# Kernel tuning notes

Hardware: AMD Instinct MI355X
Metric: run time of the kernel (lower is better)

Reference implementation:

```python
import jax, jax.numpy as jnp
import numpy as np

B, W, I, S, T, U, US = 4, 2000, 64, 64, 24, 32, 2
V, H, D, OUT = 32000, 4, 256, 512
PER = W + I + S + U + 1          # nodes per graph = 2161
N = B * PER                      # 8644 nodes
E_RAND = N * 16


def setup_inputs() -> dict:
    key = jax.random.key(0)
    ks = jax.random.split(key, 24)
    s = 0.02
    inp = {}
    inp["all_words"] = jax.random.randint(ks[0], (B * W,), 0, V)
    inp["image_feats"] = jax.random.normal(ks[1], (B * I, 2048), jnp.float32)
    inp["sentences"] = jax.random.randint(ks[2], (B, S, T), 0, V)
    inp["sentence_mask"] = jnp.ones((B, S, T), jnp.float32)
    inp["utterances"] = jax.random.randint(ks[3], (B, U, US), 0, S)
    inp["utterance_mask"] = jnp.ones((B, U, US), jnp.float32)
    inp["session_ids"] = (jnp.arange(B) + 1) * PER - 1   # last node of each graph
    src = jax.random.randint(ks[4], (E_RAND,), 0, N)
    dst = jax.random.randint(ks[5], (E_RAND,), 0, N)
    loop = jnp.arange(N)
    inp["edge_src"] = jnp.concatenate([src, loop])
    inp["edge_dst"] = jnp.concatenate([dst, loop])
    # learned parameters
    inp["word_embed"] = jax.random.normal(ks[6], (V, 300), jnp.float32) * s
    inp["text_fc_w"] = jax.random.normal(ks[7], (300, 1024), jnp.float32) * s
    inp["text_fc_b"] = jnp.zeros((1024,), jnp.float32)
    inp["image_fc_w"] = jax.random.normal(ks[8], (2048, 1024), jnp.float32) * s
    inp["image_fc_b"] = jnp.zeros((1024,), jnp.float32)
    inp["gat0_fc"] = jax.random.normal(ks[9], (1024, H * D), jnp.float32) * s
    inp["gat0_al"] = jax.random.normal(ks[10], (H, D), jnp.float32) * s
    inp["gat0_ar"] = jax.random.normal(ks[11], (H, D), jnp.float32) * s
    inp["gat0_b"] = jnp.zeros((H * D,), jnp.float32)
    inp["gat1_fc"] = jax.random.normal(ks[12], (H * D, H * D), jnp.float32) * s
    inp["gat1_al"] = jax.random.normal(ks[13], (H, D), jnp.float32) * s
    inp["gat1_ar"] = jax.random.normal(ks[14], (H, D), jnp.float32) * s
    inp["gat1_b"] = jnp.zeros((H * D,), jnp.float32)
    inp["gat2_fc"] = jax.random.normal(ks[15], (H * D, OUT), jnp.float32) * s
    inp["gat2_al"] = jax.random.normal(ks[16], (1, OUT), jnp.float32) * s
    inp["gat2_ar"] = jax.random.normal(ks[17], (1, OUT), jnp.float32) * s
    inp["gat2_b"] = jnp.zeros((OUT,), jnp.float32)
    return inp


def _gat_layer(h, src, dst, fc_w, al, ar, b, act):
    # DGL GATConv: fc -> per-head attention logits -> edge softmax over dst -> aggregate
    n = h.shape[0]
    nh, dd = al.shape
    f = (h @ fc_w).reshape(n, nh, dd)                    # [N,H,D]
    el = (f * al).sum(-1)                                # [N,H]
    er = (f * ar).sum(-1)
    e = jax.nn.leaky_relu(el[src] + er[dst], 0.2)        # [E,H]
    m = jax.ops.segment_max(e, dst, num_segments=n)      # stable softmax per dst node
    a = jnp.exp(e - m[dst])
    z = jax.ops.segment_sum(a, dst, num_segments=n)
    alpha = a / z[dst]                                   # [E,H]
    out = jax.ops.segment_sum(alpha[:, :, None] * f[src], dst, num_segments=n)
    out = out + b.reshape(nh, dd)
    if act:
        out = jax.nn.elu(out)
    return out.reshape(n, nh * dd)


def _masked_mean(x, mask):
    # x: [..., K, F], mask: [..., K]
    s = (x * mask[..., None]).sum(-2)
    cnt = mask.sum(-1, keepdims=True)
    cnt = jnp.where(cnt == 0, 1.0, cnt)
    return s / cnt


def reference(all_words, image_feats, sentences, sentence_mask, utterances,
              utterance_mask, session_ids, edge_src, edge_dst,
              word_embed, text_fc_w, text_fc_b, image_fc_w, image_fc_b,
              gat0_fc, gat0_al, gat0_ar, gat0_b,
              gat1_fc, gat1_al, gat1_ar, gat1_b,
              gat2_fc, gat2_al, gat2_ar, gat2_b):
    b, s_num, t_num = sentences.shape
    u_num, us_num = utterances.shape[1], utterances.shape[2]
    w_per = all_words.shape[0] // b
    i_per = image_feats.shape[0] // b

    # word nodes
    we = word_embed[all_words].reshape(b, w_per, 300)
    # sentence nodes: masked mean over words
    sw = word_embed[sentences]                           # [B,S,T,300]
    sent = _masked_mean(sw, sentence_mask)               # [B,S,300]
    # utterance nodes: gather sentence embeds, masked mean over sentences
    uidx = utterances.reshape(b, u_num * us_num)
    ue = jnp.take_along_axis(sent, uidx[:, :, None], axis=1).reshape(b, u_num, us_num, -1)
    utt = _masked_mean(ue, utterance_mask)               # [B,U,300]
    # session node
    sess = utt.mean(axis=1, keepdims=True)               # [B,1,300]

    txt = lambda x: x @ text_fc_w + text_fc_b
    wf, sf, uf, ssf = txt(we), txt(sent), txt(utt), txt(sess)
    imf = (image_feats @ image_fc_w + image_fc_b).reshape(b, i_per, -1)

    # node layout per graph: [words, images, sentences, utterances, session]
    h = jnp.concatenate([wf, imf, sf, uf, ssf], axis=1).reshape(-1, 1024)

    h = _gat_layer(h, edge_src, edge_dst, gat0_fc, gat0_al, gat0_ar, gat0_b, act=True)
    h = _gat_layer(h, edge_src, edge_dst, gat1_fc, gat1_al, gat1_ar, gat1_b, act=True)
    h = _gat_layer(h, edge_src, edge_dst, gat2_fc, gat2_al, gat2_ar, gat2_b, act=False)

    return h[session_ids]                                # [B, 512]
```

## Files before the change

kernel.cpp:

```cpp
#include <hip/hip_runtime.h>
#include <math.h>

constexpr int kB = 4, kW = 2000, kI = 64, kS = 64, kT = 24, kU = 32, kUS = 2;
constexpr int kPER = kW + kI + kS + kU + 1;
constexpr int kN   = kB * kPER;
constexpr int kTxtPer  = kW + kS + kU + 1;
constexpr int kTxtRows = kB * kTxtPer;
constexpr int kEmb = 300;
constexpr int kEmbPad = 320;
constexpr int kHid = 1024;
constexpr int kOut = 512;
constexpr int kCap = 256;
constexpr int kMaxDeg = 256;

typedef __attribute__((ext_vector_type(8))) short bf16x8;
typedef __attribute__((ext_vector_type(4))) float f32x4;

__device__ __forceinline__ unsigned short f2bf(float f) {
  union { float f; unsigned int u; } x; x.f = f;
  unsigned int r = x.u + 0x7FFF + ((x.u >> 16) & 1);
  return (unsigned short)(r >> 16);
}
__device__ __forceinline__ float bf2f(unsigned short u) {
  union { unsigned int u; float f; } x; x.u = ((unsigned int)u) << 16;
  return x.f;
}


__global__ void k_sent(const int* __restrict__ sents, const float* __restrict__ smask,
                       const float* __restrict__ wemb, float* __restrict__ sent) {
  int bs = blockIdx.x;
  __shared__ int idx[kT];
  __shared__ float mk[kT];
  __shared__ float s_cnt;
  int t = threadIdx.x;
  if (t < kT) { idx[t] = sents[bs * kT + t]; mk[t] = smask[bs * kT + t]; }
  __syncthreads();
  if (t == 0) {
    float c = 0.f;
    for (int i = 0; i < kT; ++i) c += mk[i];
    s_cnt = (c == 0.f) ? 1.f : c;
  }
  __syncthreads();
  for (int d = t; d < kEmb; d += blockDim.x) {
    float acc = 0.f;
    for (int i = 0; i < kT; ++i) acc += wemb[idx[i] * kEmb + d] * mk[i];
    sent[bs * kEmb + d] = acc / s_cnt;
  }
}

__global__ void k_utt(const int* __restrict__ utts, const float* __restrict__ umask,
                      const float* __restrict__ sent, float* __restrict__ utt) {
  int bu = blockIdx.x;
  int b = bu / kU;
  __shared__ int idx[kUS];
  __shared__ float mk[kUS];
  __shared__ float s_cnt;
  int t = threadIdx.x;
  if (t < kUS) { idx[t] = utts[bu * kUS + t]; mk[t] = umask[bu * kUS + t]; }
  __syncthreads();
  if (t == 0) {
    float c = 0.f;
    for (int i = 0; i < kUS; ++i) c += mk[i];
    s_cnt = (c == 0.f) ? 1.f : c;
  }
  __syncthreads();
  for (int d = t; d < kEmb; d += blockDim.x) {
    float acc = 0.f;
    for (int i = 0; i < kUS; ++i) acc += sent[(b * kS + idx[i]) * kEmb + d] * mk[i];
    utt[bu * kEmb + d] = acc / s_cnt;
  }
}

__global__ void k_sess(const float* __restrict__ utt, float* __restrict__ sess) {
  int b = blockIdx.x;
  for (int d = threadIdx.x; d < kEmb; d += blockDim.x) {
    float acc = 0.f;
    for (int u = 0; u < kU; ++u) acc += utt[(b * kU + u) * kEmb + d];
    sess[b * kEmb + d] = acc * (1.f / kU);
  }
}

__global__ void k_txtgather(const int* __restrict__ aw, const float* __restrict__ wemb,
                            const float* __restrict__ sent, const float* __restrict__ utt,
                            const float* __restrict__ sess, unsigned short* __restrict__ txt) {
  int r = blockIdx.x;
  int g = r / kTxtPer, j = r - g * kTxtPer;
  const float* src;
  if (j < kW)                 src = wemb + (size_t)aw[g * kW + j] * kEmb;
  else if (j < kW + kS)       src = sent + (size_t)(g * kS + (j - kW)) * kEmb;
  else if (j < kW + kS + kU)  src = utt  + (size_t)(g * kU + (j - kW - kS)) * kEmb;
  else                        src = sess + (size_t)g * kEmb;
  for (int d = threadIdx.x; d < kEmbPad; d += blockDim.x)
    txt[(size_t)r * kEmbPad + d] = (d < kEmb) ? f2bf(src[d]) : (unsigned short)0;
}

__global__ void k_rowmap(int* __restrict__ rt, int* __restrict__ ri) {
  int i = blockIdx.x * blockDim.x + threadIdx.x;
  if (i < kTxtRows) {
    int g = i / kTxtPer, j = i - g * kTxtPer;
    int base = g * kPER;
    int node;
    if (j < kW)                 node = base + j;
    else if (j < kW + kS)       node = base + kW + kI + (j - kW);
    else if (j < kW + kS + kU)  node = base + kW + kI + kS + (j - kW - kS);
    else                        node = base + kW + kI + kS + kU;
    rt[i] = node;
  }
  if (i < kB * kI) {
    int g = i >> 6;
    ri[i] = g * kPER + kW + (i & 63);
  }
}

__global__ void k_prep(const float* __restrict__ tx_w, unsigned short* __restrict__ o_tx,
                       const float* __restrict__ im_w, unsigned short* __restrict__ o_im,
                       const float* __restrict__ g0_w, unsigned short* __restrict__ o_g0,
                       const float* __restrict__ g1_w, unsigned short* __restrict__ o_g1,
                       const float* __restrict__ g2_w, unsigned short* __restrict__ o_g2,
                       const float* __restrict__ img, unsigned short* __restrict__ o_img) {
  int b = blockIdx.x;
  int tx = threadIdx.x, ty = threadIdx.y;
  const float* in; unsigned short* out; int K, N, Kpad, nbx;
  if (b < 320)               { in = tx_w; out = o_tx; K = kEmb; N = kHid; Kpad = kEmbPad; nbx = 32; }
  else if ((b -= 320) < 2048){ in = im_w; out = o_im; K = 2048; N = kHid; Kpad = 2048; nbx = 32; }
  else if ((b -= 2048) < 1024){ in = g0_w; out = o_g0; K = kHid; N = kHid; Kpad = kHid; nbx = 32; }
  else if ((b -= 1024) < 1024){ in = g1_w; out = o_g1; K = kHid; N = kHid; Kpad = kHid; nbx = 32; }
  else if ((b -= 1024) < 512) { in = g2_w; out = o_g2; K = kHid; N = kOut; Kpad = kHid; nbx = 16; }
  else {
    int i = (b - 512) * 1024 + (ty * 32 + tx) * 4;
    float4 v = *(const float4*)(img + i);
    ushort4 o; o.x = f2bf(v.x); o.y = f2bf(v.y); o.z = f2bf(v.z); o.w = f2bf(v.w);
    *(ushort4*)(o_img + i) = o;
    return;
  }
  int bx = b % nbx, by = b / nbx;
  __shared__ float t[32][33];
  int n = bx * 32 + tx;
#pragma unroll
  for (int j = 0; j < 4; ++j) {
    int k = by * 32 + ty + j * 8;
    t[ty + j * 8][tx] = (k < K) ? in[(size_t)k * N + n] : 0.f;
  }
  __syncthreads();
#pragma unroll
  for (int j = 0; j < 4; ++j) {
    int nn = bx * 32 + ty + j * 8;
    int kk = by * 32 + tx;
    out[(size_t)nn * Kpad + kk] = f2bf(t[tx][ty + j * 8]);
  }
}

template <bool OBF>
__global__ __launch_bounds__(256) void k_mm2(const unsigned short* __restrict__ A,
                                             const unsigned short* __restrict__ Bt,
                                             const float* __restrict__ bias,
                                             const int* __restrict__ rmap,
                                             void* __restrict__ Cout,
                                             int M, int K, int Nc) {
  __shared__ __align__(16) unsigned short As[128 * 64];
  __shared__ __align__(16) unsigned short Bs[128 * 64];
  int nCol = Nc >> 7;
  int bi = blockIdx.x;
  int xcd = bi & 7, bj = bi >> 3;
  int colTile = bj % nCol;
  int rowTile = ((bj / nCol) << 3) + xcd;
  int row0 = rowTile << 7;
  if (row0 >= M) return;
  int col0 = colTile << 7;

  int tid = threadIdx.x;
  int wid = tid >> 6, lane = tid & 63, quad = lane >> 4, l16 = lane & 15;
  int wm = wid >> 1, wn = wid & 1;

  f32x4 acc[4][4];
  f32x4 zero4 = {0.f, 0.f, 0.f, 0.f};
#pragma unroll
  for (int i = 0; i < 4; ++i)
#pragma unroll
    for (int j = 0; j < 4; ++j) acc[i][j] = zero4;

  int ar_ = tid >> 3;
  int ac = tid & 7;

  for (int k0 = 0; k0 < K; k0 += 64) {
    __syncthreads();
#pragma unroll
    for (int i = 0; i < 4; ++i) {
      int r = ar_ + i * 32;
      int sw = ((ac ^ (r & 7)) << 3);
      int grow = row0 + r;
      uint4 va = make_uint4(0u, 0u, 0u, 0u);
      if (grow < M) va = *(const uint4*)(A + (size_t)grow * K + k0 + ac * 8);
      *(uint4*)&As[r * 64 + sw] = va;
      int nrow = col0 + r;
      uint4 vb = *(const uint4*)(Bt + (size_t)nrow * K + k0 + ac * 8);
      *(uint4*)&Bs[r * 64 + sw] = vb;
    }
    __syncthreads();
#pragma unroll
    for (int s = 0; s < 2; ++s) {
      int cc = s * 4 + quad;
      bf16x8 aF[4], bF[4];
#pragma unroll
      for (int mi = 0; mi < 4; ++mi) {
        int r = wm * 64 + mi * 16 + l16;
        aF[mi] = *(const bf16x8*)&As[r * 64 + ((cc ^ (r & 7)) << 3)];
      }
#pragma unroll
      for (int ni = 0; ni < 4; ++ni) {
        int r = wn * 64 + ni * 16 + l16;
        bF[ni] = *(const bf16x8*)&Bs[r * 64 + ((cc ^ (r & 7)) << 3)];
      }
#pragma unroll
      for (int mi = 0; mi < 4; ++mi)
#pragma unroll
        for (int ni = 0; ni < 4; ++ni)
          acc[mi][ni] = __builtin_amdgcn_mfma_f32_16x16x32_bf16(aF[mi], bF[ni], acc[mi][ni], 0, 0, 0);
    }
  }

#pragma unroll
  for (int mi = 0; mi < 4; ++mi) {
#pragma unroll
    for (int ni = 0; ni < 4; ++ni) {
      int gm0 = row0 + wm * 64 + mi * 16 + quad * 4;
      int gn  = col0 + wn * 64 + ni * 16 + l16;
      float bv = bias ? bias[gn] : 0.f;
#pragma unroll
      for (int i = 0; i < 4; ++i) {
        int r = gm0 + i;
        if (r >= M) continue;
        float v = acc[mi][ni][i] + bv;
        if (OBF) {
          int orow = rmap ? rmap[r] : r;
          ((unsigned short*)Cout)[(size_t)orow * Nc + gn] = f2bf(v);
        } else {
          ((float*)Cout)[(size_t)r * Nc + gn] = v;
        }
      }
    }
  }
}

__global__ void k_elr4(const unsigned short* __restrict__ f, const float* __restrict__ al,
                       const float* __restrict__ ar, float* __restrict__ el,
                       float* __restrict__ er) {
  int v = blockIdx.x;
  int h = threadIdx.x >> 6, lane = threadIdx.x & 63;
  int d = lane * 4;
  ushort4 fv = *(const ushort4*)(f + (size_t)v * 1024 + h * 256 + d);
  float4 av = *(const float4*)(al + h * 256 + d);
  float4 rv = *(const float4*)(ar + h * 256 + d);
  float x0 = bf2f(fv.x), x1 = bf2f(fv.y), x2 = bf2f(fv.z), x3 = bf2f(fv.w);
  float a = x0 * av.x + x1 * av.y + x2 * av.z + x3 * av.w;
  float b = x0 * rv.x + x1 * rv.y + x2 * rv.z + x3 * rv.w;
#pragma unroll
  for (int off = 32; off; off >>= 1) {
    a += __shfl_down(a, off);
    b += __shfl_down(b, off);
  }
  if (lane == 0) { el[v * 4 + h] = a; er[v * 4 + h] = b; }
}

__global__ __launch_bounds__(256) void k_mm_sk(const unsigned short* __restrict__ A,
                                               const unsigned short* __restrict__ Bt,
                                               const int* __restrict__ rowlist,
                                               float* __restrict__ C,
                                               int M, int K, int Nc, int Kc) {
  __shared__ __align__(16) unsigned short As[64 * 64];
  __shared__ __align__(16) unsigned short Bs[64 * 64];
  int tid = threadIdx.x;
  int wid = tid >> 6, lane = tid & 63, quad = lane >> 4, l16 = lane & 15;
  int row0 = blockIdx.y * 64, col0 = blockIdx.x * 64;
  int k0 = blockIdx.z * Kc;
  int k1 = k0 + Kc; if (k1 > K) k1 = K;

  f32x4 acc[4];
  f32x4 zero4 = {0.f, 0.f, 0.f, 0.f};
#pragma unroll
  for (int i = 0; i < 4; ++i) acc[i] = zero4;

  int ar_ = tid >> 3;
  int ac = tid & 7;

  for (int kk = k0; kk < k1; kk += 64) {
    __syncthreads();
#pragma unroll
    for (int i = 0; i < 2; ++i) {
      int r = ar_ + i * 32;
      int sw = ((ac ^ (r & 7)) << 3);
      int grow = row0 + r;
      uint4 va = make_uint4(0u, 0u, 0u, 0u);
      if (grow < M) {
        int arow = rowlist ? rowlist[grow] : grow;
        va = *(const uint4*)(A + (size_t)arow * K + kk + ac * 8);
      }
      *(uint4*)&As[r * 64 + sw] = va;
      int nrow = col0 + r;
      uint4 vb = *(const uint4*)(Bt + (size_t)nrow * K + kk + ac * 8);
      *(uint4*)&Bs[r * 64 + sw] = vb;
    }
    __syncthreads();
#pragma unroll
    for (int s = 0; s < 2; ++s) {
      int cc = s * 4 + quad;
      bf16x8 bF;
      {
        int r = wid * 16 + l16;
        bF = *(const bf16x8*)&Bs[r * 64 + ((cc ^ (r & 7)) << 3)];
      }
#pragma unroll
      for (int mi = 0; mi < 4; ++mi) {
        int r = mi * 16 + l16;
        bf16x8 aF = *(const bf16x8*)&As[r * 64 + ((cc ^ (r & 7)) << 3)];
        acc[mi] = __builtin_amdgcn_mfma_f32_16x16x32_bf16(aF, bF, acc[mi], 0, 0, 0);
      }
    }
  }
#pragma unroll
  for (int mi = 0; mi < 4; ++mi) {
#pragma unroll
    for (int i = 0; i < 4; ++i) {
      int r = row0 + mi * 16 + quad * 4 + i;
      int c = col0 + wid * 16 + l16;
      if (r < M) atomicAdd(&C[(size_t)r * Nc + c], acc[mi][i]);
    }
  }
}

__global__ void k_sk_epi(const float* __restrict__ Cw, const float* __restrict__ bias,
                         const int* __restrict__ rmap, unsigned short* __restrict__ out,
                         int M, int Nc) {
  int i = blockIdx.x * blockDim.x + threadIdx.x;
  if (i >= M * Nc) return;
  int r = i / Nc, c = i - r * Nc;
  out[(size_t)rmap[r] * Nc + c] = f2bf(Cw[i] + bias[c]);
}

__global__ void k_count(const int* __restrict__ dst, int* __restrict__ cnt, int E) {
  int e = blockIdx.x * blockDim.x + threadIdx.x;
  if (e < E) atomicAdd(&cnt[dst[e]], 1);
}

__global__ void k_scan(const int* __restrict__ deg, int* __restrict__ offs, int n) {
  __shared__ int part[1024];
  int tid = threadIdx.x;
  int per = (n + 1023) >> 10;
  int start = tid * per;
  int local = 0;
  for (int i = 0; i < per; ++i) { int idx = start + i; if (idx < n) local += deg[idx]; }
  part[tid] = local;
  __syncthreads();
  for (int off = 1; off < 1024; off <<= 1) {
    int add = (tid >= off) ? part[tid - off] : 0;
    __syncthreads();
    part[tid] += add;
    __syncthreads();
  }
  int run = (tid == 0) ? 0 : part[tid - 1];
  for (int i = 0; i < per; ++i) {
    int idx = start + i;
    if (idx < n) { offs[idx] = run; run += deg[idx]; }
  }
  if (tid == 1023) offs[n] = part[1023];
}

__global__ void k_fill(const int* __restrict__ src, const int* __restrict__ dst,
                       const int* __restrict__ offs, int* __restrict__ cur,
                       int* __restrict__ csr, int E) {
  int e = blockIdx.x * blockDim.x + threadIdx.x;
  if (e < E) {
    int d = dst[e];
    int slot = offs[d] + atomicAdd(&cur[d], 1);
    csr[slot] = src[e];
  }
}

__global__ __launch_bounds__(256) void k_agg3(const unsigned short* __restrict__ f,
                                              const float* __restrict__ el,
                                              const float* __restrict__ er,
                                              const int* __restrict__ offs,
                                              const int* __restrict__ csr,
                                              const float* __restrict__ bias,
                                              unsigned short* __restrict__ out) {
  __shared__ float xs[4][kMaxDeg];
  int v = blockIdx.x;
  int tid = threadIdx.x;
  int h = tid >> 6, lane = tid & 63;
  int e0 = offs[v];
  int deg = offs[v + 1] - e0;
  if (deg > kMaxDeg) deg = kMaxDeg;

  float erv = er[v * 4 + h];
  float m = -1e30f;
  for (int base = 0; base < deg; base += 64) {
    int idx = base + lane;
    float x = -1e30f;
    if (idx < deg) {
      int s = csr[e0 + idx];
      x = el[s * 4 + h] + erv;
      x = x > 0.f ? x : 0.2f * x;
      xs[h][idx] = x;
    }
    float mm = x;
#pragma unroll
    for (int o = 32; o; o >>= 1) mm = fmaxf(mm, __shfl_xor(mm, o));
    m = fmaxf(m, mm);
  }
  float zs = 0.f;
  for (int base = 0; base < deg; base += 64) {
    int idx = base + lane;
    if (idx < deg) {
      float w = expf(xs[h][idx] - m);
      xs[h][idx] = w;
      zs += w;
    }
  }
#pragma unroll
  for (int o = 32; o; o >>= 1) zs += __shfl_xor(zs, o);
  float rz = 1.f / zs;
  for (int base = 0; base < deg; base += 64) {
    int idx = base + lane;
    if (idx < deg) xs[h][idx] *= rz;
  }
  __syncthreads();

  int d0 = tid * 4;
  float a0 = 0.f, a1 = 0.f, a2 = 0.f, a3 = 0.f;
  for (int e = 0; e < deg; ++e) {
    int s = csr[e0 + e];
    float w = xs[h][e];
    ushort4 fv = *(const ushort4*)(f + (size_t)s * 1024 + d0);
    a0 += w * bf2f(fv.x);
    a1 += w * bf2f(fv.y);
    a2 += w * bf2f(fv.z);
    a3 += w * bf2f(fv.w);
  }
  float4 bv = *(const float4*)(bias + d0);
  float o0 = a0 + bv.x, o1 = a1 + bv.y, o2 = a2 + bv.z, o3 = a3 + bv.w;
  o0 = o0 > 0.f ? o0 : expm1f(o0);
  o1 = o1 > 0.f ? o1 : expm1f(o1);
  o2 = o2 > 0.f ? o2 : expm1f(o2);
  o3 = o3 > 0.f ? o3 : expm1f(o3);
  ushort4 ov;
  ov.x = f2bf(o0); ov.y = f2bf(o1); ov.z = f2bf(o2); ov.w = f2bf(o3);
  *(ushort4*)(out + (size_t)v * 1024 + d0) = ov;
}

__global__ void k_rows2(const int* __restrict__ sid, const int* __restrict__ offs,
                        const int* __restrict__ csr, int* __restrict__ rowlist,
                        int* __restrict__ info) {
  __shared__ int degs[kB], starts[kB], total;
  int tid = threadIdx.x;
  int bv = tid >> 6, lane = tid & 63;
  if (tid < kB) {
    int v = sid[tid];
    degs[tid] = offs[v + 1] - offs[v];
  }
  __syncthreads();
  if (tid == 0) {
    int p = 0;
    for (int b = 0; b < kB; ++b) {
      starts[b] = p;
      int d = degs[b];
      if (p + d > kCap) d = kCap - p;
      degs[b] = d;
      p += d;
    }
    total = p;
  }
  __syncthreads();
  int v = sid[bv];
  int e0 = offs[v];
  int deg = degs[bv];
  int start = starts[bv];
  if (lane == 0) {
    info[bv] = start;
    info[4 + bv] = deg;
    info[8 + bv] = start;
  }
  __syncthreads();
  for (int idx = lane; idx < deg; idx += 64) {
    int s = csr[e0 + idx];
    rowlist[start + idx] = s;
    if (s == v) info[8 + bv] = start + idx;
  }
  for (int i = total + tid; i < kCap; i += 256) rowlist[i] = 0;
}

__global__ void k_elr_c(const float* __restrict__ fc, const float* __restrict__ al,
                        const float* __restrict__ ar, float* __restrict__ el,
                        float* __restrict__ er) {
  int r = blockIdx.x;
  int lane = threadIdx.x;
  float a = 0.f, b = 0.f;
  for (int d = lane * 4; d < 512; d += 256) {
    float4 x = *(const float4*)(fc + (size_t)r * 512 + d);
    float4 av = *(const float4*)(al + d);
    float4 rv = *(const float4*)(ar + d);
    a += x.x * av.x + x.y * av.y + x.z * av.z + x.w * av.w;
    b += x.x * rv.x + x.y * rv.y + x.z * rv.z + x.w * rv.w;
  }
#pragma unroll
  for (int off = 32; off; off >>= 1) {
    a += __shfl_down(a, off);
    b += __shfl_down(b, off);
  }
  if (lane == 0) { el[r] = a; er[r] = b; }
}

__global__ __launch_bounds__(256) void k_agg_fin2(const float* __restrict__ fc,
                                                  const float* __restrict__ el,
                                                  const float* __restrict__ er,
                                                  const int* __restrict__ info,
                                                  const float* __restrict__ bias,
                                                  float* __restrict__ out) {
  int bv = blockIdx.x;
  int tid = threadIdx.x;
  int start = info[bv], cnt = info[4 + bv];
  float erv = er[info[8 + bv]];
  float m = -1e30f;
  for (int i = 0; i < cnt; ++i) {
    float x = el[start + i] + erv;
    x = x > 0.f ? x : 0.2f * x;
    m = fmaxf(m, x);
  }
  float z = 0.f, a0 = 0.f, a1 = 0.f;
  for (int i = 0; i < cnt; ++i) {
    int r = start + i;
    float x = el[r] + erv;
    x = x > 0.f ? x : 0.2f * x;
    float w = expf(x - m);
    z += w;
    a0 += w * fc[(size_t)r * 512 + tid];
    a1 += w * fc[(size_t)r * 512 + 256 + tid];
  }
  out[bv * 512 + tid] = a0 / z + bias[tid];
  out[bv * 512 + 256 + tid] = a1 / z + bias[256 + tid];
}

extern "C" void kernel_launch(void* const* d_in, const int* in_sizes, int n_in,
                              void* d_out, int out_size, void* d_ws, size_t ws_size,
                              hipStream_t stream) {
  const int*   all_words   = (const int*)d_in[0];
  const float* image_feats = (const float*)d_in[1];
  const int*   sentences   = (const int*)d_in[2];
  const float* sent_mask   = (const float*)d_in[3];
  const int*   utterances  = (const int*)d_in[4];
  const float* utt_mask    = (const float*)d_in[5];
  const int*   session_ids = (const int*)d_in[6];
  const int*   edge_src    = (const int*)d_in[7];
  const int*   edge_dst    = (const int*)d_in[8];
  const float* word_embed  = (const float*)d_in[9];
  const float* text_fc_w   = (const float*)d_in[10];
  const float* text_fc_b   = (const float*)d_in[11];
  const float* image_fc_w  = (const float*)d_in[12];
  const float* image_fc_b  = (const float*)d_in[13];
  const float* gat0_fc     = (const float*)d_in[14];
  const float* gat0_al     = (const float*)d_in[15];
  const float* gat0_ar     = (const float*)d_in[16];
  const float* gat0_b      = (const float*)d_in[17];
  const float* gat1_fc     = (const float*)d_in[18];
  const float* gat1_al     = (const float*)d_in[19];
  const float* gat1_ar     = (const float*)d_in[20];
  const float* gat1_b      = (const float*)d_in[21];
  const float* gat2_fc     = (const float*)d_in[22];
  const float* gat2_al     = (const float*)d_in[23];
  const float* gat2_ar     = (const float*)d_in[24];
  const float* gat2_b      = (const float*)d_in[25];

  const int E = in_sizes[7];

  char* base = (char*)d_ws;
  size_t off = 0;
  auto alloc = [&](size_t elems, size_t esz) -> void* {
    void* p = base + off;
    off += ((elems * esz + 255) / 256) * 256;
    return p;
  };
  unsigned short* Abf   = (unsigned short*)alloc((size_t)kN * kHid, 2);
  unsigned short* fbf   = (unsigned short*)alloc((size_t)kN * kHid, 2);
  unsigned short* txtbf = (unsigned short*)alloc((size_t)kTxtRows * kEmbPad, 2);
  unsigned short* imgbf = (unsigned short*)alloc((size_t)kB * kI * 2048, 2);
  unsigned short* wtTx  = (unsigned short*)alloc((size_t)kHid * kEmbPad, 2);
  unsigned short* wtIm  = (unsigned short*)alloc((size_t)kHid * 2048, 2);
  unsigned short* wtG0  = (unsigned short*)alloc((size_t)kHid * kHid, 2);
  unsigned short* wtG1  = (unsigned short*)alloc((size_t)kHid * kHid, 2);
  unsigned short* wtG2  = (unsigned short*)alloc((size_t)kOut * kHid, 2);
  float* Cimg   = (float*)alloc((size_t)kB * kI * kHid, 4);
  float* Cg2    = (float*)alloc((size_t)kCap * kOut, 4);
  float* sentb  = (float*)alloc((size_t)kB * kS * kEmb, 4);
  float* uttb   = (float*)alloc((size_t)kB * kU * kEmb, 4);
  float* sessb  = (float*)alloc((size_t)kB * kEmb, 4);
  float* el     = (float*)alloc((size_t)kN * 4, 4);
  float* er     = (float*)alloc((size_t)kN * 4, 4);
  int*   offs   = (int*)alloc(kN + 1, 4);
  int*   cnt    = (int*)alloc(kN, 4);
  int*   csr    = (int*)alloc(E, 4);
  int*   rmt    = (int*)alloc(kTxtRows, 4);
  int*   rmi    = (int*)alloc(kB * kI, 4);
  int*   rowl   = (int*)alloc(kCap, 4);
  int*   info   = (int*)alloc(16, 4);
  (void)ws_size; (void)n_in; (void)out_size;

  k_sent<<<kB * kS, 128, 0, stream>>>(sentences, sent_mask, word_embed, sentb);
  k_utt<<<kB * kU, 128, 0, stream>>>(utterances, utt_mask, sentb, uttb);
  k_sess<<<kB, 128, 0, stream>>>(uttb, sessb);
  k_txtgather<<<kTxtRows, 128, 0, stream>>>(all_words, word_embed, sentb, uttb, sessb, txtbf);
  k_rowmap<<<(kTxtRows + 255) / 256, 256, 0, stream>>>(rmt, rmi);
  k_prep<<<5440, dim3(32, 8), 0, stream>>>(text_fc_w, wtTx, image_fc_w, wtIm,
                                           gat0_fc, wtG0, gat1_fc, wtG1, gat2_fc, wtG2,
                                           image_feats, imgbf);

  hipMemsetAsync(cnt, 0, kN * sizeof(int), stream);
  k_count<<<(E + 255) / 256, 256, 0, stream>>>(edge_dst, cnt, E);
  k_scan<<<1, 1024, 0, stream>>>(cnt, offs, kN);
  hipMemsetAsync(cnt, 0, kN * sizeof(int), stream);
  k_fill<<<(E + 255) / 256, 256, 0, stream>>>(edge_src, edge_dst, offs, cnt, csr, E);

  auto mmGrid = [](int M, int Nc) {
    int nrt = (M + 127) / 128;
    return 8 * (Nc / 128) * ((nrt + 7) / 8);
  };

  k_mm2<true><<<mmGrid(kTxtRows, kHid), 256, 0, stream>>>(
      txtbf, wtTx, text_fc_b, rmt, Abf, kTxtRows, kEmbPad, kHid);

  hipMemsetAsync(Cimg, 0, (size_t)kB * kI * kHid * sizeof(float), stream);
  k_mm_sk<<<dim3(kHid / 64, kB * kI / 64, 4), 256, 0, stream>>>(
      imgbf, wtIm, nullptr, Cimg, kB * kI, 2048, kHid, 512);
  k_sk_epi<<<(kB * kI * kHid + 255) / 256, 256, 0, stream>>>(
      Cimg, image_fc_b, rmi, Abf, kB * kI, kHid);

  k_mm2<true><<<mmGrid(kN, kHid), 256, 0, stream>>>(
      Abf, wtG0, nullptr, nullptr, fbf, kN, kHid, kHid);
  k_elr4<<<kN, 256, 0, stream>>>(fbf, gat0_al, gat0_ar, el, er);
  k_agg3<<<kN, 256, 0, stream>>>(fbf, el, er, offs, csr, gat0_b, Abf);

  k_mm2<true><<<mmGrid(kN, kHid), 256, 0, stream>>>(
      Abf, wtG1, nullptr, nullptr, fbf, kN, kHid, kHid);
  k_elr4<<<kN, 256, 0, stream>>>(fbf, gat1_al, gat1_ar, el, er);
  k_agg3<<<kN, 256, 0, stream>>>(fbf, el, er, offs, csr, gat1_b, Abf);

  k_rows2<<<1, 256, 0, stream>>>(session_ids, offs, csr, rowl, info);
  hipMemsetAsync(Cg2, 0, (size_t)kCap * kOut * sizeof(float), stream);
  k_mm_sk<<<dim3(kOut / 64, kCap / 64, 4), 256, 0, stream>>>(
      Abf, wtG2, rowl, Cg2, kCap, kHid, kOut, 256);
  k_elr_c<<<kCap, 64, 0, stream>>>(Cg2, gat2_al, gat2_ar, el, er);
  k_agg_fin2<<<kB, 256, 0, stream>>>(Cg2, el, er, info, gat2_b, (float*)d_out);
}
```

Measured before the change: 444.0 us.

## Fold attention projections into GEMM columns and merge small setup kernels

Precomputes W·a_l and W·a_r as eight extra weight columns so the GAT layer-0/1 GEMMs emit el/er directly, removing the separate k_elr4 passes over the features. Merges the sentence, rowmap, memset and weight-prep work into one large prep kernel, fuses utterance/session and text-gather/edge-count kernels, and moves the count reset into the scan. This cuts launch count and one read of the feature matrix per layer. In exchange the GEMMs gain a ninth column tile that is mostly padding, and el/er are computed from bf16 weights instead of bf16 features, which changes rounding.

```diff
diff --git a/kernel.cpp b/kernel.cpp
--- a/kernel.cpp
+++ b/kernel.cpp
@@ -12,6 +12,7 @@
 constexpr int kOut = 512;
 constexpr int kCap = 256;
 constexpr int kMaxDeg = 256;
+constexpr int kNcB = 1152;
 
 typedef __attribute__((ext_vector_type(8))) short bf16x8;
 typedef __attribute__((ext_vector_type(4))) float f32x4;
@@ -26,114 +27,105 @@
   return x.f;
 }
 
-
-__global__ void k_sent(const int* __restrict__ sents, const float* __restrict__ smask,
-                       const float* __restrict__ wemb, float* __restrict__ sent) {
-  int bs = blockIdx.x;
-  __shared__ int idx[kT];
-  __shared__ float mk[kT];
-  __shared__ float s_cnt;
-  int t = threadIdx.x;
-  if (t < kT) { idx[t] = sents[bs * kT + t]; mk[t] = smask[bs * kT + t]; }
-  __syncthreads();
-  if (t == 0) {
-    float c = 0.f;
-    for (int i = 0; i < kT; ++i) c += mk[i];
-    s_cnt = (c == 0.f) ? 1.f : c;
-  }
-  __syncthreads();
-  for (int d = t; d < kEmb; d += blockDim.x) {
-    float acc = 0.f;
-    for (int i = 0; i < kT; ++i) acc += wemb[idx[i] * kEmb + d] * mk[i];
-    sent[bs * kEmb + d] = acc / s_cnt;
-  }
-}
-
-__global__ void k_utt(const int* __restrict__ utts, const float* __restrict__ umask,
-                      const float* __restrict__ sent, float* __restrict__ utt) {
-  int bu = blockIdx.x;
-  int b = bu / kU;
-  __shared__ int idx[kUS];
-  __shared__ float mk[kUS];
-  __shared__ float s_cnt;
-  int t = threadIdx.x;
-  if (t < kUS) { idx[t] = utts[bu * kUS + t]; mk[t] = umask[bu * kUS + t]; }
-  __syncthreads();
-  if (t == 0) {
-    float c = 0.f;
-    for (int i = 0; i < kUS; ++i) c += mk[i];
-    s_cnt = (c == 0.f) ? 1.f : c;
-  }
-  __syncthreads();
-  for (int d = t; d < kEmb; d += blockDim.x) {
-    float acc = 0.f;
-    for (int i = 0; i < kUS; ++i) acc += sent[(b * kS + idx[i]) * kEmb + d] * mk[i];
-    utt[bu * kEmb + d] = acc / s_cnt;
-  }
-}
-
-__global__ void k_sess(const float* __restrict__ utt, float* __restrict__ sess) {
+__global__ __launch_bounds__(256) void k_prep0(
+    const float* __restrict__ tx_w, unsigned short* __restrict__ o_tx,
+    const float* __restrict__ im_w, unsigned short* __restrict__ o_im,
+    const float* __restrict__ g0_w, unsigned short* __restrict__ o_g0,
+    const float* __restrict__ g1_w, unsigned short* __restrict__ o_g1,
+    const float* __restrict__ g2_w, unsigned short* __restrict__ o_g2,
+    const float* __restrict__ img, unsigned short* __restrict__ o_img,
+    const int* __restrict__ sents, const float* __restrict__ smask,
+    const float* __restrict__ wemb, float* __restrict__ sent,
+    int* __restrict__ rmt, int* __restrict__ rmi,
+    int* __restrict__ cnt, float* __restrict__ Cimg, float* __restrict__ Cg2,
+    const float* __restrict__ g0_al, const float* __restrict__ g0_ar,
+    const float* __restrict__ g1_al, const float* __restrict__ g1_ar) {
   int b = blockIdx.x;
-  for (int d = threadIdx.x; d < kEmb; d += blockDim.x) {
-    float acc = 0.f;
-    for (int u = 0; u < kU; ++u) acc += utt[(b * kU + u) * kEmb + d];
-    sess[b * kEmb + d] = acc * (1.f / kU);
-  }
-}
-
-__global__ void k_txtgather(const int* __restrict__ aw, const float* __restrict__ wemb,
-                            const float* __restrict__ sent, const float* __restrict__ utt,
-                            const float* __restrict__ sess, unsigned short* __restrict__ txt) {
-  int r = blockIdx.x;
-  int g = r / kTxtPer, j = r - g * kTxtPer;
-  const float* src;
-  if (j < kW)                 src = wemb + (size_t)aw[g * kW + j] * kEmb;
-  else if (j < kW + kS)       src = sent + (size_t)(g * kS + (j - kW)) * kEmb;
-  else if (j < kW + kS + kU)  src = utt  + (size_t)(g * kU + (j - kW - kS)) * kEmb;
-  else                        src = sess + (size_t)g * kEmb;
-  for (int d = threadIdx.x; d < kEmbPad; d += blockDim.x)
-    txt[(size_t)r * kEmbPad + d] = (d < kEmb) ? f2bf(src[d]) : (unsigned short)0;
-}
-
-__global__ void k_rowmap(int* __restrict__ rt, int* __restrict__ ri) {
-  int i = blockIdx.x * blockDim.x + threadIdx.x;
-  if (i < kTxtRows) {
-    int g = i / kTxtPer, j = i - g * kTxtPer;
-    int base = g * kPER;
-    int node;
-    if (j < kW)                 node = base + j;
-    else if (j < kW + kS)       node = base + kW + kI + (j - kW);
-    else if (j < kW + kS + kU)  node = base + kW + kI + kS + (j - kW - kS);
-    else                        node = base + kW + kI + kS + kU;
-    rt[i] = node;
-  }
-  if (i < kB * kI) {
-    int g = i >> 6;
-    ri[i] = g * kPER + kW + (i & 63);
-  }
-}
-
-__global__ void k_prep(const float* __restrict__ tx_w, unsigned short* __restrict__ o_tx,
-                       const float* __restrict__ im_w, unsigned short* __restrict__ o_im,
-                       const float* __restrict__ g0_w, unsigned short* __restrict__ o_g0,
-                       const float* __restrict__ g1_w, unsigned short* __restrict__ o_g1,
-                       const float* __restrict__ g2_w, unsigned short* __restrict__ o_g2,
-                       const float* __restrict__ img, unsigned short* __restrict__ o_img) {
-  int b = blockIdx.x;
-  int tx = threadIdx.x, ty = threadIdx.y;
-  const float* in; unsigned short* out; int K, N, Kpad, nbx;
-  if (b < 320)               { in = tx_w; out = o_tx; K = kEmb; N = kHid; Kpad = kEmbPad; nbx = 32; }
-  else if ((b -= 320) < 2048){ in = im_w; out = o_im; K = 2048; N = kHid; Kpad = 2048; nbx = 32; }
+  int tid = threadIdx.x;
+  int tx = tid & 31, ty = tid >> 5;
+
+  const float* in = nullptr; unsigned short* out = nullptr; int K = 0, N = 0, Kpad = 0, nbx = 0;
+  if (b < 320)                { in = tx_w; out = o_tx; K = kEmb; N = kHid; Kpad = kEmbPad; nbx = 32; }
+  else if ((b -= 320) < 2048) { in = im_w; out = o_im; K = 2048; N = kHid; Kpad = 2048; nbx = 32; }
   else if ((b -= 2048) < 1024){ in = g0_w; out = o_g0; K = kHid; N = kHid; Kpad = kHid; nbx = 32; }
   else if ((b -= 1024) < 1024){ in = g1_w; out = o_g1; K = kHid; N = kHid; Kpad = kHid; nbx = 32; }
   else if ((b -= 1024) < 512) { in = g2_w; out = o_g2; K = kHid; N = kOut; Kpad = kHid; nbx = 16; }
-  else {
-    int i = (b - 512) * 1024 + (ty * 32 + tx) * 4;
+  else if ((b -= 512) < 512) {
+    int i = b * 1024 + tid * 4;
     float4 v = *(const float4*)(img + i);
     ushort4 o; o.x = f2bf(v.x); o.y = f2bf(v.y); o.z = f2bf(v.z); o.w = f2bf(v.w);
     *(ushort4*)(o_img + i) = o;
     return;
-  }
+  } else if ((b -= 512) < 256) {
+    __shared__ int idx[kT];
+    __shared__ float mk[kT];
+    __shared__ float s_cnt;
+    if (tid < kT) { idx[tid] = sents[b * kT + tid]; mk[tid] = smask[b * kT + tid]; }
+    __syncthreads();
+    if (tid == 0) {
+      float c = 0.f;
+      for (int i = 0; i < kT; ++i) c += mk[i];
+      s_cnt = (c == 0.f) ? 1.f : c;
+    }
+    __syncthreads();
+    for (int d = tid; d < kEmb; d += 256) {
+      float acc = 0.f;
+      for (int i = 0; i < kT; ++i) acc += wemb[idx[i] * kEmb + d] * mk[i];
+      sent[b * kEmb + d] = acc / s_cnt;
+    }
+    return;
+  } else if ((b -= 256) < 34) {
+    int i = b * 256 + tid;
+    if (i < kTxtRows) {
+      int g = i / kTxtPer, j = i - g * kTxtPer;
+      int base = g * kPER;
+      int node;
+      if (j < kW)                 node = base + j;
+      else if (j < kW + kS)       node = base + kW + kI + (j - kW);
+      else if (j < kW + kS + kU)  node = base + kW + kI + kS + (j - kW - kS);
+      else                        node = base + kW + kI + kS + kU;
+      rmt[i] = node;
+    }
+    if (i < kB * kI) {
+      int g = i >> 6;
+      rmi[i] = g * kPER + kW + (i & 63);
+    }
+    return;
+  } else if ((b -= 34) < 34) {
+    int i = b * 256 + tid;
+    if (i < kN) cnt[i] = 0;
+    return;
+  } else if ((b -= 34) < 256) {
+    uint4 z = make_uint4(0u, 0u, 0u, 0u);
+    ((uint4*)Cimg)[b * 256 + tid] = z;
+    return;
+  } else if ((b -= 256) < 128) {
+    uint4 z = make_uint4(0u, 0u, 0u, 0u);
+    ((uint4*)Cg2)[b * 256 + tid] = z;
+    return;
+  } else if ((b -= 128) < 8) {
+    int layer = b >> 2, which = (b >> 1) & 1, kslab = b & 1;
+    const float* fc = layer ? g1_w : g0_w;
+    const float* a  = layer ? (which ? g1_ar : g1_al) : (which ? g0_ar : g0_al);
+    unsigned short* wt = layer ? o_g1 : o_g0;
+    for (int k = kslab * 512 + tid; k < kslab * 512 + 512; k += 256) {
+#pragma unroll
+      for (int h = 0; h < 4; ++h) {
+        float s = 0.f;
+        for (int d = 0; d < 256; ++d) s += fc[(size_t)k * kHid + h * 256 + d] * a[h * 256 + d];
+        wt[(size_t)(1024 + which * 4 + h) * kHid + k] = f2bf(s);
+      }
+    }
+    return;
+  } else {
+    b -= 8;
+    int i = b * 256 + tid;
+    uint4 z = make_uint4(0u, 0u, 0u, 0u);
+    ((uint4*)(o_g0 + (size_t)1032 * kHid))[i] = z;
+    ((uint4*)(o_g1 + (size_t)1032 * kHid))[i] = z;
+    return;
+  }
+
   int bx = b % nbx, by = b / nbx;
   __shared__ float t[32][33];
   int n = bx * 32 + tx;
@@ -151,16 +143,90 @@
   }
 }
 
-template <bool OBF>
+__global__ __launch_bounds__(256) void k_utt_sess(const int* __restrict__ utts,
+                                                  const float* __restrict__ umask,
+                                                  const float* __restrict__ sent,
+                                                  float* __restrict__ utt,
+                                                  float* __restrict__ sess) {
+  int blk = blockIdx.x;
+  int tid = threadIdx.x;
+  if (blk < kB * kU) {
+    int bu = blk, b = bu / kU;
+    __shared__ int idx[kUS];
+    __shared__ float mk[kUS];
+    __shared__ float s_cnt;
+    if (tid < kUS) { idx[tid] = utts[bu * kUS + tid]; mk[tid] = umask[bu * kUS + tid]; }
+    __syncthreads();
+    if (tid == 0) {
+      float c = 0.f;
+      for (int i = 0; i < kUS; ++i) c += mk[i];
+      s_cnt = (c == 0.f) ? 1.f : c;
+    }
+    __syncthreads();
+    for (int d = tid; d < kEmb; d += 256) {
+      float acc = 0.f;
+      for (int i = 0; i < kUS; ++i) acc += sent[(b * kS + idx[i]) * kEmb + d] * mk[i];
+      utt[bu * kEmb + d] = acc / s_cnt;
+    }
+  } else {
+    int b = blk - kB * kU;
+    for (int d = tid; d < kEmb; d += 256) {
+      float acc = 0.f;
+      for (int u = 0; u < kU; ++u) {
+        float ua = 0.f, c = 0.f;
+        for (int us = 0; us < kUS; ++us) {
+          int i = (b * kU + u) * kUS + us;
+          int sidx = utts[i];
+          float m = umask[i];
+          ua += sent[(b * kS + sidx) * kEmb + d] * m;
+          c += m;
+        }
+        if (c == 0.f) c = 1.f;
+        acc += ua / c;
+      }
+      sess[b * kEmb + d] = acc * (1.f / kU);
+    }
+  }
+}
+
+__global__ __launch_bounds__(256) void k_txtcount(const int* __restrict__ aw,
+                                                  const float* __restrict__ wemb,
+                                                  const float* __restrict__ sent,
+                                                  const float* __restrict__ utt,
+                                                  const float* __restrict__ sess,
+                                                  unsigned short* __restrict__ txt,
+                                                  const int* __restrict__ dst,
+                                                  int* __restrict__ cnt, int E) {
+  int blk = blockIdx.x;
+  int tid = threadIdx.x;
+  if (blk < kTxtRows) {
+    int r = blk;
+    int g = r / kTxtPer, j = r - g * kTxtPer;
+    const float* src;
+    if (j < kW)                 src = wemb + (size_t)aw[g * kW + j] * kEmb;
+    else if (j < kW + kS)       src = sent + (size_t)(g * kS + (j - kW)) * kEmb;
+    else if (j < kW + kS + kU)  src = utt  + (size_t)(g * kU + (j - kW - kS)) * kEmb;
+    else                        src = sess + (size_t)g * kEmb;
+    for (int d = tid; d < kEmbPad; d += 256)
+      txt[(size_t)r * kEmbPad + d] = (d < kEmb) ? f2bf(src[d]) : (unsigned short)0;
+  } else {
+    int e = (blk - kTxtRows) * 256 + tid;
+    if (e < E) atomicAdd(&cnt[dst[e]], 1);
+  }
+}
+
+template <bool OBF, bool ELR>
 __global__ __launch_bounds__(256) void k_mm2(const unsigned short* __restrict__ A,
                                              const unsigned short* __restrict__ Bt,
                                              const float* __restrict__ bias,
                                              const int* __restrict__ rmap,
                                              void* __restrict__ Cout,
-                                             int M, int K, int Nc) {
+                                             float* __restrict__ el,
+                                             float* __restrict__ er,
+                                             int M, int K, int NcB, int NcOut) {
   __shared__ __align__(16) unsigned short As[128 * 64];
   __shared__ __align__(16) unsigned short Bs[128 * 64];
-  int nCol = Nc >> 7;
+  int nCol = NcB >> 7;
   int bi = blockIdx.x;
   int xcd = bi & 7, bj = bi >> 3;
   int colTile = bj % nCol;
@@ -226,41 +292,27 @@
     for (int ni = 0; ni < 4; ++ni) {
       int gm0 = row0 + wm * 64 + mi * 16 + quad * 4;
       int gn  = col0 + wn * 64 + ni * 16 + l16;
-      float bv = bias ? bias[gn] : 0.f;
+      float bv = (bias && gn < NcOut) ? bias[gn] : 0.f;
 #pragma unroll
       for (int i = 0; i < 4; ++i) {
         int r = gm0 + i;
         if (r >= M) continue;
         float v = acc[mi][ni][i] + bv;
-        if (OBF) {
-          int orow = rmap ? rmap[r] : r;
-          ((unsigned short*)Cout)[(size_t)orow * Nc + gn] = f2bf(v);
-        } else {
-          ((float*)Cout)[(size_t)r * Nc + gn] = v;
+        if (gn < NcOut) {
+          if (OBF) {
+            int orow = rmap ? rmap[r] : r;
+            ((unsigned short*)Cout)[(size_t)orow * NcOut + gn] = f2bf(v);
+          } else {
+            ((float*)Cout)[(size_t)r * NcOut + gn] = v;
+          }
+        } else if (ELR) {
+          int gn2 = gn - NcOut;
+          if (gn2 < 4)      el[r * 4 + gn2] = v;
+          else if (gn2 < 8) er[r * 4 + gn2 - 4] = v;
         }
       }
     }
   }
-}
-
-__global__ void k_elr4(const unsigned short* __restrict__ f, const float* __restrict__ al,
-                       const float* __restrict__ ar, float* __restrict__ el,
-                       float* __restrict__ er) {
-  int v = blockIdx.x;
-  int h = threadIdx.x >> 6, lane = threadIdx.x & 63;
-  int d = lane * 4;
-  ushort4 fv = *(const ushort4*)(f + (size_t)v * 1024 + h * 256 + d);
-  float4 av = *(const float4*)(al + h * 256 + d);
-  float4 rv = *(const float4*)(ar + h * 256 + d);
-  float x0 = bf2f(fv.x), x1 = bf2f(fv.y), x2 = bf2f(fv.z), x3 = bf2f(fv.w);
-  float a = x0 * av.x + x1 * av.y + x2 * av.z + x3 * av.w;
-  float b = x0 * rv.x + x1 * rv.y + x2 * rv.z + x3 * rv.w;
-#pragma unroll
-  for (int off = 32; off; off >>= 1) {
-    a += __shfl_down(a, off);
-    b += __shfl_down(b, off);
-  }
-  if (lane == 0) { el[v * 4 + h] = a; er[v * 4 + h] = b; }
 }
 
 __global__ __launch_bounds__(256) void k_mm_sk(const unsigned short* __restrict__ A,
@@ -338,12 +390,7 @@
   out[(size_t)rmap[r] * Nc + c] = f2bf(Cw[i] + bias[c]);
 }
 
-__global__ void k_count(const int* __restrict__ dst, int* __restrict__ cnt, int E) {
-  int e = blockIdx.x * blockDim.x + threadIdx.x;
-  if (e < E) atomicAdd(&cnt[dst[e]], 1);
-}
-
-__global__ void k_scan(const int* __restrict__ deg, int* __restrict__ offs, int n) {
+__global__ void k_scan(int* __restrict__ deg, int* __restrict__ offs, int n) {
   __shared__ int part[1024];
   int tid = threadIdx.x;
   int per = (n + 1023) >> 10;
@@ -364,6 +411,8 @@
     if (idx < n) { offs[idx] = run; run += deg[idx]; }
   }
   if (tid == 1023) offs[n] = part[1023];
+  __syncthreads();
+  for (int i = tid; i < n; i += 1024) deg[i] = 0;
 }
 
 __global__ void k_fill(const int* __restrict__ src, const int* __restrict__ dst,
@@ -585,8 +634,8 @@
   unsigned short* imgbf = (unsigned short*)alloc((size_t)kB * kI * 2048, 2);
   unsigned short* wtTx  = (unsigned short*)alloc((size_t)kHid * kEmbPad, 2);
   unsigned short* wtIm  = (unsigned short*)alloc((size_t)kHid * 2048, 2);
-  unsigned short* wtG0  = (unsigned short*)alloc((size_t)kHid * kHid, 2);
-  unsigned short* wtG1  = (unsigned short*)alloc((size_t)kHid * kHid, 2);
+  unsigned short* wtG0  = (unsigned short*)alloc((size_t)kNcB * kHid, 2);
+  unsigned short* wtG1  = (unsigned short*)alloc((size_t)kNcB * kHid, 2);
   unsigned short* wtG2  = (unsigned short*)alloc((size_t)kOut * kHid, 2);
   float* Cimg   = (float*)alloc((size_t)kB * kI * kHid, 4);
   float* Cg2    = (float*)alloc((size_t)kCap * kOut, 4);
@@ -604,47 +653,42 @@
   int*   info   = (int*)alloc(16, 4);
   (void)ws_size; (void)n_in; (void)out_size;
 
-  k_sent<<<kB * kS, 128, 0, stream>>>(sentences, sent_mask, word_embed, sentb);
-  k_utt<<<kB * kU, 128, 0, stream>>>(utterances, utt_mask, sentb, uttb);
-  k_sess<<<kB, 128, 0, stream>>>(uttb, sessb);
-  k_txtgather<<<kTxtRows, 128, 0, stream>>>(all_words, word_embed, sentb, uttb, sessb, txtbf);
-  k_rowmap<<<(kTxtRows + 255) / 256, 256, 0, stream>>>(rmt, rmi);
-  k_prep<<<5440, dim3(32, 8), 0, stream>>>(text_fc_w, wtTx, image_fc_w, wtIm,
-                                           gat0_fc, wtG0, gat1_fc, wtG1, gat2_fc, wtG2,
-                                           image_feats, imgbf);
-
-  hipMemsetAsync(cnt, 0, kN * sizeof(int), stream);
-  k_count<<<(E + 255) / 256, 256, 0, stream>>>(edge_dst, cnt, E);
+  constexpr int kPrepBlocks = 320 + 2048 + 1024 + 1024 + 512 + 512 + 256 + 34 + 34 + 256 + 128 + 8 + 60;
+  k_prep0<<<kPrepBlocks, 256, 0, stream>>>(
+      text_fc_w, wtTx, image_fc_w, wtIm, gat0_fc, wtG0, gat1_fc, wtG1, gat2_fc, wtG2,
+      image_feats, imgbf, sentences, sent_mask, word_embed, sentb, rmt, rmi,
+      cnt, Cimg, Cg2, gat0_al, gat0_ar, gat1_al, gat1_ar);
+
+  k_utt_sess<<<kB * kU + kB, 256, 0, stream>>>(utterances, utt_mask, sentb, uttb, sessb);
+
+  k_txtcount<<<kTxtRows + (E + 255) / 256, 256, 0, stream>>>(
+      all_words, word_embed, sentb, uttb, sessb, txtbf, edge_dst, cnt, E);
+
   k_scan<<<1, 1024, 0, stream>>>(cnt, offs, kN);
-  hipMemsetAsync(cnt, 0, kN * sizeof(int), stream);
   k_fill<<<(E + 255) / 256, 256, 0, stream>>>(edge_src, edge_dst, offs, cnt, csr, E);
 
-  auto mmGrid = [](int M, int Nc) {
+  auto mmGrid = [](int M, int NcB_) {
     int nrt = (M + 127) / 128;
-    return 8 * (Nc / 128) * ((nrt + 7) / 8);
+    return 8 * (NcB_ / 128) * ((nrt + 7) / 8);
   };
 
-  k_mm2<true><<<mmGrid(kTxtRows, kHid), 256, 0, stream>>>(
-      txtbf, wtTx, text_fc_b, rmt, Abf, kTxtRows, kEmbPad, kHid);
-
-  hipMemsetAsync(Cimg, 0, (size_t)kB * kI * kHid * sizeof(float), stream);
+  k_mm2<true, false><<<mmGrid(kTxtRows, kHid), 256, 0, stream>>>(
+      txtbf, wtTx, text_fc_b, rmt, Abf, nullptr, nullptr, kTxtRows, kEmbPad, kHid, kHid);
+
   k_mm_sk<<<dim3(kHid / 64, kB * kI / 64, 4), 256, 0, stream>>>(
       imgbf, wtIm, nullptr, Cimg, kB * kI, 2048, kHid, 512);
   k_sk_epi<<<(kB * kI * kHid + 255) / 256, 256, 0, stream>>>(
       Cimg, image_fc_b, rmi, Abf, kB * kI, kHid);
 
-  k_mm2<true><<<mmGrid(kN, kHid), 256, 0, stream>>>(
-      Abf, wtG0, nullptr, nullptr, fbf, kN, kHid, kHid);
-  k_elr4<<<kN, 256, 0, stream>>>(fbf, gat0_al, gat0_ar, el, er);
+  k_mm2<true, true><<<mmGrid(kN, kNcB), 256, 0, stream>>>(
+      Abf, wtG0, nullptr, nullptr, fbf, el, er, kN, kHid, kNcB, kHid);
   k_agg3<<<kN, 256, 0, stream>>>(fbf, el, er, offs, csr, gat0_b, Abf);
 
-  k_mm2<true><<<mmGrid(kN, kHid), 256, 0, stream>>>(
-      Abf, wtG1, nullptr, nullptr, fbf, kN, kHid, kHid);
-  k_elr4<<<kN, 256, 0, stream>>>(fbf, gat1_al, gat1_ar, el, er);
+  k_mm2<true, true><<<mmGrid(kN, kNcB), 256, 0, stream>>>(
+      Abf, wtG1, nullptr, nullptr, fbf, el, er, kN, kHid, kNcB, kHid);
   k_agg3<<<kN, 256, 0, stream>>>(fbf, el, er, offs, csr, gat1_b, Abf);
 
   k_rows2<<<1, 256, 0, stream>>>(session_ids, offs, csr, rowl, info);
-  hipMemsetAsync(Cg2, 0, (size_t)kCap * kOut * sizeof(float), stream);
   k_mm_sk<<<dim3(kOut / 64, kCap / 64, 4), 256, 0, stream>>>(
       Abf, wtG2, rowl, Cg2, kCap, kHid, kOut, 256);
   k_elr_c<<<kCap, 64, 0, stream>>>(Cg2, gat2_al, gat2_ar, el, er);
```

Result: slower. 480.7 us (+8.3%).
